# Kernel tuning notes

Measured on AMD Instinct MI355X. Metric: run time of the kernel, lower is better.

## Reference

```python
import jax, jax.numpy as jnp
import numpy as np

N_NODES = 100000
N_EDGES = 1000000
F_DIM = 128


def setup_inputs() -> dict:
    key = jax.random.key(0)
    ks = jax.random.split(key, 12)
    s = lambda k, shape: jax.random.normal(k, shape, dtype=jnp.float32) * (1.0 / np.sqrt(shape[0]))
    return {
        "x": jax.random.normal(ks[0], (N_NODES, F_DIM), dtype=jnp.float32),
        "edge_index": jax.random.randint(ks[1], (2, N_EDGES), 0, N_NODES, dtype=jnp.int64),
        "W1": s(ks[2], (2 * F_DIM, 64)), "b1": jnp.zeros((64,), jnp.float32), "A1": s(ks[3], (2 * F_DIM, 64)),
        "W2": s(ks[4], (64, 32)), "b2": jnp.zeros((32,), jnp.float32), "A2": s(ks[5], (64, 32)),
        "W3": s(ks[6], (32, 16)), "b3": jnp.zeros((16,), jnp.float32), "A3": s(ks[7], (32, 16)),
        "Wf": s(ks[8], (16, 1)), "bf": jnp.zeros((1,), jnp.float32),
    }


def _res_block(h, W, b, A):
    # out = relu(h @ W + b); residual = h @ A (bias-free adjust); return relu(out + residual)
    out = jax.nn.relu(h @ W + b)
    return jax.nn.relu(out + h @ A)


def reference(x, edge_index, W1, b1, A1, W2, b2, A2, W3, b3, A3, Wf, bf):
    # NOTE: in the original forward, the GNN output is overwritten by data.x,
    # so the effective computation is gather -> concat -> residual MLP -> sigmoid.
    src, dst = edge_index[0], edge_index[1]
    h = jnp.concatenate([x[src], x[dst]], axis=-1)  # [E, 2F]
    h = _res_block(h, W1, b1, A1)  # [E, 64]
    h = _res_block(h, W2, b2, A2)  # [E, 32]
    h = _res_block(h, W3, b3, A3)  # [E, 16]
    return jax.nn.sigmoid(h @ Wf + bf)  # [E, 1]
```

## Files before the change

kernel.cpp:

```cpp
#include <hip/hip_runtime.h>
#include <stdint.h>

#define E_TOTAL 1000000
#define FD      128
#define ETILE   64
#define NTILES  (E_TOTAL / ETILE)
#define GRID    1024

typedef __attribute__((ext_vector_type(8))) short short8;
typedef __attribute__((ext_vector_type(4))) short short4v;
typedef __attribute__((ext_vector_type(4))) float f32x4;

__device__ __forceinline__ short f2bf(float f) {
  union { float f; unsigned u; } v; v.f = f;
  unsigned r = (v.u + 0x7FFFu + ((v.u >> 16) & 1u)) >> 16;
  return (short)(r & 0xFFFFu);
}

__global__ __launch_bounds__(256, 2)
void linkpred_kernel(const float* __restrict__ x,
                     const int* __restrict__ ei,
                     const float* __restrict__ W1, const float* __restrict__ b1,
                     const float* __restrict__ A1,
                     const float* __restrict__ W2, const float* __restrict__ b2,
                     const float* __restrict__ A2,
                     const float* __restrict__ W3, const float* __restrict__ b3,
                     const float* __restrict__ A3,
                     const float* __restrict__ Wf, const float* __restrict__ bfp,
                     float* __restrict__ out)
{
  __shared__ __align__(16) short H0[ETILE][264];
  __shared__ __align__(16) short H1[ETILE][72];
  __shared__ __align__(16) short H2[ETILE][40];
  __shared__ float H3[ETILE][17];
  __shared__ int   SIDX[2][ETILE];

  const int tid  = threadIdx.x;
  const int w    = tid >> 6;
  const int lane = tid & 63;
  const int col  = lane & 15;
  const int quad = lane >> 4;

  short8 B1f[2][8];
  for (int p = 0; p < 2; ++p) {
    const int n = 16 * (w + 4 * p) + col;
    const float* src = (p == 0) ? (W1 + n) : (A1 + (n - 64));
    for (int kt = 0; kt < 8; ++kt) {
      short8 f;
      for (int j = 0; j < 8; ++j)
        f[j] = f2bf(src[(kt * 32 + quad * 8 + j) * 64]);
      B1f[p][kt] = f;
    }
  }
  short8 B2f[2][2];
  for (int p = 0; p < 2; ++p) {
    const int n = 16 * ((w & 1) + 2 * p) + col;
    const float* src = (p == 0) ? (W2 + n) : (A2 + (n - 32));
    for (int kt = 0; kt < 2; ++kt) {
      short8 f;
      for (int j = 0; j < 8; ++j)
        f[j] = f2bf(src[(kt * 32 + quad * 8 + j) * 32]);
      B2f[p][kt] = f;
    }
  }
  short8 B3f[2];
  for (int p = 0; p < 2; ++p) {
    const int n = 16 * p + col;
    const float* src = (p == 0) ? (W3 + n) : (A3 + (n - 16));
    short8 f;
    for (int j = 0; j < 8; ++j)
      f[j] = f2bf(src[(quad * 8 + j) * 16]);
    B3f[p] = f;
  }
  const float b1v = b1[16 * w + col];
  const float b2v = b2[16 * (w & 1) + col];
  const float b3v = b3[col];
  const float bfv = bfp[0];
  const f32x4 zero = {0.f, 0.f, 0.f, 0.f};

  for (int tile = blockIdx.x; tile < NTILES; tile += gridDim.x) {
    const int e0 = tile * ETILE;

    if (tid < ETILE)            SIDX[0][tid] = ei[e0 + tid];
    else if (tid < 2 * ETILE)   SIDX[1][tid - ETILE] = ei[E_TOTAL + e0 + (tid - ETILE)];
    __syncthreads();

    for (int it = 0; it < ETILE / 4; ++it) {
      const int e    = it * 4 + w;
      const int node = SIDX[lane >> 5][e];
      const int cc   = lane & 31;
      float4 v = ((const float4*)(x + (size_t)node * FD))[cc];
      short4v s;
      s[0] = f2bf(v.x); s[1] = f2bf(v.y); s[2] = f2bf(v.z); s[3] = f2bf(v.w);
      *(short4v*)&H0[e][lane * 4] = s;
    }
    __syncthreads();

    f32x4 acc[4][2];
    for (int mt = 0; mt < 4; ++mt) { acc[mt][0] = zero; acc[mt][1] = zero; }
    for (int kt = 0; kt < 8; ++kt) {
      for (int mt = 0; mt < 4; ++mt) {
        short8 a = *(const short8*)&H0[mt * 16 + col][kt * 32 + quad * 8];
        acc[mt][0] = __builtin_amdgcn_mfma_f32_16x16x32_bf16(a, B1f[0][kt], acc[mt][0], 0, 0, 0);
        acc[mt][1] = __builtin_amdgcn_mfma_f32_16x16x32_bf16(a, B1f[1][kt], acc[mt][1], 0, 0, 0);
      }
    }
    for (int mt = 0; mt < 4; ++mt)
      for (int r = 0; r < 4; ++r) {
        float o = fmaxf(acc[mt][0][r] + b1v, 0.f);
        float h = fmaxf(o + acc[mt][1][r], 0.f);
        H1[mt * 16 + quad * 4 + r][16 * w + col] = f2bf(h);
      }
    __syncthreads();

    f32x4 acc2[2][2];
    acc2[0][0] = zero; acc2[0][1] = zero; acc2[1][0] = zero; acc2[1][1] = zero;
    for (int kt = 0; kt < 2; ++kt)
      for (int mi = 0; mi < 2; ++mi) {
        const int m = (2 * (w >> 1) + mi) * 16 + col;
        short8 a = *(const short8*)&H1[m][kt * 32 + quad * 8];
        acc2[mi][0] = __builtin_amdgcn_mfma_f32_16x16x32_bf16(a, B2f[0][kt], acc2[mi][0], 0, 0, 0);
        acc2[mi][1] = __builtin_amdgcn_mfma_f32_16x16x32_bf16(a, B2f[1][kt], acc2[mi][1], 0, 0, 0);
      }
    for (int mi = 0; mi < 2; ++mi)
      for (int r = 0; r < 4; ++r) {
        float o = fmaxf(acc2[mi][0][r] + b2v, 0.f);
        float h = fmaxf(o + acc2[mi][1][r], 0.f);
        H2[(2 * (w >> 1) + mi) * 16 + quad * 4 + r][16 * (w & 1) + col] = f2bf(h);
      }
    __syncthreads();

    f32x4 acc3[2];
    acc3[0] = zero; acc3[1] = zero;
    {
      short8 a = *(const short8*)&H2[w * 16 + col][quad * 8];
      acc3[0] = __builtin_amdgcn_mfma_f32_16x16x32_bf16(a, B3f[0], acc3[0], 0, 0, 0);
      acc3[1] = __builtin_amdgcn_mfma_f32_16x16x32_bf16(a, B3f[1], acc3[1], 0, 0, 0);
    }
    for (int r = 0; r < 4; ++r) {
      float o = fmaxf(acc3[0][r] + b3v, 0.f);
      float h = fmaxf(o + acc3[1][r], 0.f);
      H3[w * 16 + quad * 4 + r][col] = h;
    }
    __syncthreads();

    if (tid < ETILE) {
      float s = bfv;
      for (int j = 0; j < 16; ++j) s += H3[tid][j] * Wf[j];
      out[e0 + tid] = 1.0f / (1.0f + __expf(-s));
    }
  }
}

extern "C" void kernel_launch(void* const* d_in, const int* in_sizes, int n_in,
                              void* d_out, int out_size, void* d_ws, size_t ws_size,
                              hipStream_t stream) {
  const float* x   = (const float*)d_in[0];
  const int*   ei  = (const int*)d_in[1];
  const float* W1  = (const float*)d_in[2];
  const float* b1  = (const float*)d_in[3];
  const float* A1  = (const float*)d_in[4];
  const float* W2  = (const float*)d_in[5];
  const float* b2  = (const float*)d_in[6];
  const float* A2  = (const float*)d_in[7];
  const float* W3  = (const float*)d_in[8];
  const float* b3  = (const float*)d_in[9];
  const float* A3  = (const float*)d_in[10];
  const float* Wf  = (const float*)d_in[11];
  const float* bfp = (const float*)d_in[12];

  hipLaunchKernelGGL(linkpred_kernel, dim3(GRID), dim3(256), 0, stream,
                     x, ei, W1, b1, A1, W2, b2, A2, W3, b3, A3, Wf, bfp,
                     (float*)d_out);
}
```

Measured before the change: 241.3 us.

## Prefetch next tile's node-feature gather into registers and shuffle-reduce final layer

```diff
diff --git a/kernel.cpp b/kernel.cpp
--- a/kernel.cpp
+++ b/kernel.cpp
@@ -1,14 +1,15 @@
 #include <hip/hip_runtime.h>
 #include <stdint.h>
+#include <stddef.h>
 
 #define E_TOTAL 1000000
+#define N_NODES 100000
 #define FD      128
 #define ETILE   64
 #define NTILES  (E_TOTAL / ETILE)
-#define GRID    1024
+#define GRID    768
 
 typedef __attribute__((ext_vector_type(8))) short short8;
-typedef __attribute__((ext_vector_type(4))) short short4v;
 typedef __attribute__((ext_vector_type(4))) float f32x4;
 
 __device__ __forceinline__ short f2bf(float f) {
@@ -32,8 +33,6 @@
   __shared__ __align__(16) short H0[ETILE][264];
   __shared__ __align__(16) short H1[ETILE][72];
   __shared__ __align__(16) short H2[ETILE][40];
-  __shared__ float H3[ETILE][17];
-  __shared__ int   SIDX[2][ETILE];
 
   const int tid  = threadIdx.x;
   const int w    = tid >> 6;
@@ -76,25 +75,45 @@
   const float b2v = b2[16 * (w & 1) + col];
   const float b3v = b3[col];
   const float bfv = bfp[0];
+  const float Wfv = Wf[col];
   const f32x4 zero = {0.f, 0.f, 0.f, 0.f};
+
+  float4 ga[8], gb[8];
+  auto prefetch = [&](int tile) {
+    const int e0 = tile * ETILE;
+#pragma unroll
+    for (int it = 0; it < 8; ++it) {
+      const int h    = w * 32 + it * 4 + quad;
+      const int e    = h >> 1;
+      const int half = h & 1;
+      const int node = ei[half * E_TOTAL + e0 + e];
+      const float4* s4 = ((const float4*)(x + (size_t)node * FD)) + col * 2;
+      ga[it] = s4[0];
+      gb[it] = s4[1];
+    }
+  };
+
+  prefetch(blockIdx.x);
 
   for (int tile = blockIdx.x; tile < NTILES; tile += gridDim.x) {
     const int e0 = tile * ETILE;
 
-    if (tid < ETILE)            SIDX[0][tid] = ei[e0 + tid];
-    else if (tid < 2 * ETILE)   SIDX[1][tid - ETILE] = ei[E_TOTAL + e0 + (tid - ETILE)];
+#pragma unroll
+    for (int it = 0; it < 8; ++it) {
+      const int h    = w * 32 + it * 4 + quad;
+      const int e    = h >> 1;
+      const int half = h & 1;
+      short8 s;
+      s[0] = f2bf(ga[it].x); s[1] = f2bf(ga[it].y);
+      s[2] = f2bf(ga[it].z); s[3] = f2bf(ga[it].w);
+      s[4] = f2bf(gb[it].x); s[5] = f2bf(gb[it].y);
+      s[6] = f2bf(gb[it].z); s[7] = f2bf(gb[it].w);
+      *(short8*)&H0[e][half * 128 + col * 8] = s;
+    }
     __syncthreads();
 
-    for (int it = 0; it < ETILE / 4; ++it) {
-      const int e    = it * 4 + w;
-      const int node = SIDX[lane >> 5][e];
-      const int cc   = lane & 31;
-      float4 v = ((const float4*)(x + (size_t)node * FD))[cc];
-      short4v s;
-      s[0] = f2bf(v.x); s[1] = f2bf(v.y); s[2] = f2bf(v.z); s[3] = f2bf(v.w);
-      *(short4v*)&H0[e][lane * 4] = s;
-    }
-    __syncthreads();
+    const int next = tile + gridDim.x;
+    if (next < NTILES) prefetch(next);
 
     f32x4 acc[4][2];
     for (int mt = 0; mt < 4; ++mt) { acc[mt][0] = zero; acc[mt][1] = zero; }
@@ -137,17 +156,20 @@
       acc3[0] = __builtin_amdgcn_mfma_f32_16x16x32_bf16(a, B3f[0], acc3[0], 0, 0, 0);
       acc3[1] = __builtin_amdgcn_mfma_f32_16x16x32_bf16(a, B3f[1], acc3[1], 0, 0, 0);
     }
+
+#pragma unroll
     for (int r = 0; r < 4; ++r) {
       float o = fmaxf(acc3[0][r] + b3v, 0.f);
       float h = fmaxf(o + acc3[1][r], 0.f);
-      H3[w * 16 + quad * 4 + r][col] = h;
-    }
-    __syncthreads();
-
-    if (tid < ETILE) {
-      float s = bfv;
-      for (int j = 0; j < 16; ++j) s += H3[tid][j] * Wf[j];
-      out[e0 + tid] = 1.0f / (1.0f + __expf(-s));
+      float t = h * Wfv;
+      t += __shfl_xor(t, 1, 16);
+      t += __shfl_xor(t, 2, 16);
+      t += __shfl_xor(t, 4, 16);
+      t += __shfl_xor(t, 8, 16);
+      if (col == r) {
+        float s = bfv + t;
+        out[e0 + w * 16 + quad * 4 + r] = 1.0f / (1.0f + __expf(-s));
+      }
     }
   }
 }
```

After: 281.7 us. +16.8%, slower.
